# Optimization experiments

Measured on AMD Instinct MI355X. Metric: run time of the kernel, lower is better.

The kernel has to match this reference:

```python
import jax, jax.numpy as jnp
import numpy as np

B, T, D, H, L, F = 256, 32, 1024, 8, 3, 2048
SSRC, NCOL, NTAB, NACT, NSYM = 64, 32, 16, 64, 32
HD = D // H


def setup_inputs() -> dict:
    key = jax.random.key(0)
    ks = jax.random.split(key, 40)
    n = lambda k, s, sc=0.02: jax.random.normal(k, s, jnp.float32) * sc
    inp = {}
    inp["prev_action_emb"] = jax.random.normal(ks[0], (B, T, D), jnp.float32)
    inp["encoded_src"] = jax.random.normal(ks[1], (B, SSRC, D), jnp.float32)
    inp["encoded_col"] = jax.random.normal(ks[2], (B, NCOL, D), jnp.float32)
    inp["encoded_tab"] = jax.random.normal(ks[3], (B, NTAB, D), jnp.float32)
    inp["src_mask"] = jnp.zeros((B, SSRC), jnp.int32)  # 1 = padded
    inp["symbol_ids"] = jax.random.randint(ks[4], (B, T), 0, NSYM)
    inp["view_type"] = jax.random.randint(ks[5], (B,), 0, 3)  # 0=action,1=col,2=tab
    inp["gold_action"] = jax.random.randint(ks[6], (B,), 0, NACT)
    inp["gold_col"] = jax.random.randint(ks[7], (B,), 0, NCOL)
    inp["gold_tab"] = jax.random.randint(ks[8], (B,), 0, NTAB)
    # grammar embeddings (torch nn.Embedding default ~ N(0,1))
    inp["symbol_emb"] = jax.random.normal(ks[9], (NSYM, D), jnp.float32)
    inp["action_emb"] = jax.random.normal(ks[10], (NACT, D), jnp.float32)
    # affine heads
    inp["action_aff_w"] = n(ks[11], (D, D)); inp["action_aff_b"] = jnp.zeros((D,), jnp.float32)
    inp["symbol_aff_w"] = n(ks[12], (D, D)); inp["symbol_aff_b"] = jnp.zeros((D,), jnp.float32)
    inp["col_aff_w"] = n(ks[13], (D, D)); inp["col_aff_b"] = jnp.zeros((D,), jnp.float32)
    inp["tab_aff_w"] = n(ks[14], (D, D)); inp["tab_aff_b"] = jnp.zeros((D,), jnp.float32)
    inp["tgt_lin_w"] = n(ks[15], (2 * D, D)); inp["tgt_lin_b"] = jnp.zeros((D,), jnp.float32)
    inp["out_lin_w"] = n(ks[16], (D, D)); inp["out_lin_b"] = jnp.zeros((D,), jnp.float32)
    # transformer decoder layers (q,k,v,o stacked on axis 1)
    inp["self_w"] = n(ks[17], (L, 4, D, D)); inp["self_b"] = jnp.zeros((L, 4, D), jnp.float32)
    inp["cross_w"] = n(ks[18], (L, 4, D, D)); inp["cross_b"] = jnp.zeros((L, 4, D), jnp.float32)
    inp["ffn_w1"] = n(ks[19], (L, D, F)); inp["ffn_b1"] = jnp.zeros((L, F), jnp.float32)
    inp["ffn_w2"] = n(ks[20], (L, F, D)); inp["ffn_b2"] = jnp.zeros((L, D), jnp.float32)
    inp["ln_g"] = jnp.ones((L, 3, D), jnp.float32); inp["ln_b"] = jnp.zeros((L, 3, D), jnp.float32)
    return inp


def _pe(t, d):
    pos = jnp.arange(t, dtype=jnp.float32)[:, None]
    div = jnp.exp(jnp.arange(0, d, 2, dtype=jnp.float32) * (-np.log(10000.0) / d))
    pe = jnp.zeros((t, d), jnp.float32)
    pe = pe.at[:, 0::2].set(jnp.sin(pos * div)).at[:, 1::2].set(jnp.cos(pos * div))
    return pe


def _ln(x, g, b, eps=1e-5):
    m = jnp.mean(x, -1, keepdims=True)
    v = jnp.mean((x - m) ** 2, -1, keepdims=True)
    return (x - m) / jnp.sqrt(v + eps) * g + b


def _mha(xq, xkv, w, b, pad=None):
    # w: [4, D, D] for q,k,v,o; pad: [B, Tk] bool key-padding mask
    q = (xq @ w[0] + b[0]).reshape(xq.shape[0], -1, H, HD)
    k = (xkv @ w[1] + b[1]).reshape(xkv.shape[0], -1, H, HD)
    v = (xkv @ w[2] + b[2]).reshape(xkv.shape[0], -1, H, HD)
    s = jnp.einsum("bqhd,bkhd->bhqk", q, k) / np.sqrt(HD).astype(np.float32)
    if pad is not None:
        s = jnp.where(pad[:, None, None, :], -1e9, s)
    a = jax.nn.softmax(s, -1)
    o = jnp.einsum("bhqk,bkhd->bqhd", a, v).reshape(xq.shape[0], -1, D)
    return o @ w[3] + b[3]


def reference(prev_action_emb, encoded_src, encoded_col, encoded_tab, symbol_emb, action_emb,
              action_aff_w, action_aff_b, symbol_aff_w, symbol_aff_b, col_aff_w, col_aff_b,
              tab_aff_w, tab_aff_b, tgt_lin_w, tgt_lin_b, out_lin_w, out_lin_b,
              self_w, self_b, cross_w, cross_b, ffn_w1, ffn_b1, ffn_w2, ffn_b2, ln_g, ln_b,
              src_mask, symbol_ids, view_type, gold_action, gold_col, gold_tab):
    # target embeddings: affine(prev action emb) ++ affine(symbol emb gather)
    tgt_a = prev_action_emb @ action_aff_w + action_aff_b            # [B,T,D]
    tgt_s = symbol_emb[symbol_ids] @ symbol_aff_w + symbol_aff_b     # [B,T,D]
    x = jnp.concatenate([tgt_a, tgt_s], -1) @ tgt_lin_w + tgt_lin_b  # [B,T,D]
    x = x + _pe(T, D)[None]  # positional encoding (dropout = eval identity)
    pad = src_mask.astype(bool)
    for l in range(L):  # post-LN TransformerDecoderLayer (torch default, relu FFN)
        x = _ln(x + _mha(x, x, self_w[l], self_b[l]), ln_g[l, 0], ln_b[l, 0])
        x = _ln(x + _mha(x, encoded_src, cross_w[l], cross_b[l], pad), ln_g[l, 1], ln_b[l, 1])
        ff = jax.nn.relu(x @ ffn_w1[l] + ffn_b1[l]) @ ffn_w2[l] + ffn_b2[l]
        x = _ln(x + ff, ln_g[l, 2], ln_b[l, 2])
    out = x[:, -1, :] @ out_lin_w + out_lin_b  # [B,D], last decode position
    # three routed prediction heads: affine(src) . out -> masked log_softmax
    src_a = action_emb @ action_aff_w + action_aff_b                 # [A,D]
    logp_a = jax.nn.log_softmax(out @ src_a.T, -1)                   # [B,A]
    src_c = encoded_col @ col_aff_w + col_aff_b                      # [B,Nc,D]
    logp_c = jax.nn.log_softmax(jnp.einsum("bnd,bd->bn", src_c, out), -1)
    src_t = encoded_tab @ tab_aff_w + tab_aff_b                      # [B,Nt,D]
    logp_t = jax.nn.log_softmax(jnp.einsum("bnd,bd->bn", src_t, out), -1)
    ga = jnp.take_along_axis(logp_a, gold_action[:, None], 1)[:, 0]
    gc = jnp.take_along_axis(logp_c, gold_col[:, None], 1)[:, 0]
    gt = jnp.take_along_axis(logp_t, gold_tab[:, None], 1)[:, 0]
    # grammar routing: each example's loss comes from exactly one view
    nll = -jnp.where(view_type == 0, ga, jnp.where(view_type == 1, gc, gt))  # [B]
    return nll
```

## Files before the change

### kernel.cpp

```cpp
#include <hip/hip_runtime.h>

typedef float  f32x4 __attribute__((ext_vector_type(4)));
typedef short  s16x8 __attribute__((ext_vector_type(8)));

__device__ __forceinline__ float b2f(short s) {
    return __uint_as_float(((unsigned)(unsigned short)s) << 16);
}
__device__ __forceinline__ short f2b(float f) {
    unsigned u = __float_as_uint(f);
    u = u + 0x7fffu + ((u >> 16) & 1u);
    return (short)(u >> 16);
}

__device__ __forceinline__ void gld_lds16(const short* g, short* l) {
    __builtin_amdgcn_global_load_lds(
        (const __attribute__((address_space(1))) unsigned int*)(const void*)g,
        (__attribute__((address_space(3))) unsigned int*)(void*)l,
        16, 0, 0);
}

#define S_VMCNT(N)  asm volatile("s_waitcnt vmcnt(" #N ")" ::: "memory")
#define S_LGKM0     asm volatile("s_waitcnt lgkmcnt(0)" ::: "memory")
#define SBAR        __builtin_amdgcn_s_barrier()
#define SCHED0      __builtin_amdgcn_sched_barrier(0)

template<int BM>
__global__ __launch_bounds__(512) void gemm_pipe(
    const short* __restrict__ A, const short* __restrict__ Bt,
    const float* __restrict__ bias,
    short* __restrict__ Cb,
    const short* __restrict__ res,
    const float* __restrict__ sym2, const int* __restrict__ sid,
    const float* __restrict__ pe,
    int M, int N, int K, int epi)
{
    constexpr int MF   = BM / 32;
    constexpr int ALW  = BM / 128;
    constexpr int BUFB = (BM + 256) * 64;
    __shared__ short lds[4 * (BM + 256) * 32];

    const int tid  = threadIdx.x;
    const int lane = tid & 63;
    const int wave = tid >> 6;

    int bid = blockIdx.x;
    int nwg = gridDim.x;
    if ((nwg & 7) == 0) { int q = nwg >> 3; bid = (bid & 7) * q + (bid >> 3); }
    const int nbx = N >> 8;
    const int m0 = (bid / nbx) * BM;
    const int n0 = (bid % nbx) * 256;

    const int wm = (wave >> 2) * (BM / 2);
    const int wn = (wave & 3) * 64;
    const int l15 = lane & 15, l4 = lane >> 4;

    f32x4 acc[MF][4];
#pragma unroll
    for (int m = 0; m < MF; m++)
#pragma unroll
        for (int n = 0; n < 4; n++)
#pragma unroll
            for (int j = 0; j < 4; j++) acc[m][n][j] = 0.f;

    int aoff[MF], boff[4];
#pragma unroll
    for (int m = 0; m < MF; m++) {
        int r = wm + m * 16 + l15;
        aoff[m] = r * 64 + ((l4 ^ ((r >> 1) & 3)) << 4);
    }
#pragma unroll
    for (int n = 0; n < 4; n++) {
        int r = wn + n * 16 + l15;
        boff[n] = BM * 64 + r * 64 + ((l4 ^ ((r >> 1) & 3)) << 4);
    }

    const int lrow = lane >> 2;
    const int lch  = (lane & 3) ^ ((lane >> 3) & 3);
    size_t agoff[ALW]; int aldo[ALW];
#pragma unroll
    for (int i = 0; i < ALW; i++) {
        int ar = wave * (BM / 8) + i * 16;
        agoff[i] = (size_t)(m0 + ar + lrow) * K + lch * 8;
        aldo[i]  = ar * 64;
    }
    size_t bgoff[2]; int bldo[2];
#pragma unroll
    for (int i = 0; i < 2; i++) {
        int br = wave * 32 + i * 16;
        bgoff[i] = (size_t)(n0 + br + lrow) * K + lch * 8;
        bldo[i]  = BM * 64 + br * 64;
    }

    char* lbase = (char*)lds;
    auto stage = [&](int kt) {
        char* lb = lbase + (kt & 3) * BUFB;
        const size_t ke = (size_t)kt * 32;
#pragma unroll
        for (int i = 0; i < ALW; i++)
            gld_lds16(A + agoff[i] + ke, (short*)(lb + aldo[i]));
#pragma unroll
        for (int i = 0; i < 2; i++)
            gld_lds16(Bt + bgoff[i] + ke, (short*)(lb + bldo[i]));
    };

    const int NT = K >> 5;
    stage(0); stage(1); stage(2);

    for (int t = 0; t < NT; t++) {
        if (t + 3 < NT) stage(t + 3);
        const int rem = NT - 1 - t;
        if (rem >= 3)      { if constexpr (ALW == 2) S_VMCNT(12); else S_VMCNT(9); }
        else if (rem == 2) { if constexpr (ALW == 2) S_VMCNT(8);  else S_VMCNT(6); }
        else if (rem == 1) { if constexpr (ALW == 2) S_VMCNT(4);  else S_VMCNT(3); }
        else               S_VMCNT(0);
        SCHED0; SBAR; SCHED0;

        const char* cp = lbase + (t & 3) * BUFB;
        s16x8 af[MF], bv[4];
#pragma unroll
        for (int m = 0; m < MF; m++) af[m] = *(const s16x8*)(cp + aoff[m]);
#pragma unroll
        for (int n = 0; n < 4; n++)  bv[n] = *(const s16x8*)(cp + boff[n]);
        __builtin_amdgcn_s_setprio(1);
#pragma unroll
        for (int m = 0; m < MF; m++)
#pragma unroll
            for (int n = 0; n < 4; n++)
                acc[m][n] = __builtin_amdgcn_mfma_f32_16x16x32_bf16(
                    af[m], bv[n], acc[m][n], 0, 0, 0);
        __builtin_amdgcn_s_setprio(0);
        S_LGKM0; SCHED0; SBAR; SCHED0;
    }

#pragma unroll
    for (int m = 0; m < MF; m++) {
#pragma unroll
        for (int n = 0; n < 4; n++) {
#pragma unroll
            for (int j = 0; j < 4; j++) {
                int row = m0 + wm + m * 16 + l4 * 4 + j;
                int col = n0 + wn + n * 16 + l15;
                float v = acc[m][n][j];
                if (bias) v += bias[col];
                size_t idx = (size_t)row * N + col;
                if (epi == 0) {
                    Cb[idx] = f2b(v);
                } else if (epi == 2) {
                    v += sym2[(size_t)sid[row] * 1024 + col] + pe[(size_t)(row & 31) * 1024 + col];
                    Cb[idx] = f2b(v);
                } else if (epi == 3) {
                    Cb[idx] = f2b(fmaxf(v, 0.f));
                } else {
                    Cb[idx] = f2b(v + b2f(res[idx]));
                }
            }
        }
    }
}

__global__ __launch_bounds__(256) void gemm_bt(
    const short* __restrict__ A, const short* __restrict__ Bt,
    const float* __restrict__ bias,
    float* __restrict__ Cf, short* __restrict__ Cb,
    const short* __restrict__ res,
    int M, int N, int K, int epi)
{
    __shared__ short As[128 * 64];
    __shared__ short Bs[128 * 64];
    const int tid  = threadIdx.x;
    const int lane = tid & 63;
    const int wave = tid >> 6;
    const int m0 = blockIdx.y * 128, n0 = blockIdx.x * 128;
    const int wm = (wave >> 1) * 64, wn = (wave & 1) * 64;
    const int l15 = lane & 15, l4 = lane >> 4;

    f32x4 acc[4][4];
#pragma unroll
    for (int m = 0; m < 4; m++)
#pragma unroll
        for (int n = 0; n < 4; n++)
#pragma unroll
            for (int j = 0; j < 4; j++) acc[m][n][j] = 0.f;

    const int srow = wave * 32 + (lane >> 3);
    const int scol = (lane & 7) * 8;
    const short* Ag = A  + (size_t)(m0 + srow) * K + scol;
    const short* Bg = Bt + (size_t)(n0 + srow) * K + scol;
    short* Al = As + (wave * 32) * 64;
    short* Bl = Bs + (wave * 32) * 64;

    for (int k0 = 0; k0 < K; k0 += 64) {
#pragma unroll
        for (int i = 0; i < 4; i++) {
            gld_lds16(Ag + (size_t)(i * 8) * K + k0, Al + i * 8 * 64);
            gld_lds16(Bg + (size_t)(i * 8) * K + k0, Bl + i * 8 * 64);
        }
        __syncthreads();
#pragma unroll
        for (int kk = 0; kk < 64; kk += 32) {
            s16x8 af[4], bfv[4];
#pragma unroll
            for (int m = 0; m < 4; m++)
                af[m] = *(const s16x8*)(As + (wm + m * 16 + l15) * 64 + kk + l4 * 8);
#pragma unroll
            for (int n = 0; n < 4; n++)
                bfv[n] = *(const s16x8*)(Bs + (wn + n * 16 + l15) * 64 + kk + l4 * 8);
#pragma unroll
            for (int m = 0; m < 4; m++)
#pragma unroll
                for (int n = 0; n < 4; n++)
                    acc[m][n] = __builtin_amdgcn_mfma_f32_16x16x32_bf16(
                        af[m], bfv[n], acc[m][n], 0, 0, 0);
        }
        __syncthreads();
    }

#pragma unroll
    for (int m = 0; m < 4; m++) {
#pragma unroll
        for (int n = 0; n < 4; n++) {
#pragma unroll
            for (int j = 0; j < 4; j++) {
                int row = m0 + wm + m * 16 + l4 * 4 + j;
                int col = n0 + wn + n * 16 + l15;
                float v = acc[m][n][j];
                if (bias) v += bias[col];
                size_t idx = (size_t)row * N + col;
                if (epi == 0) {
                    Cb[idx] = f2b(v);
                } else if (epi == 1) {
                    Cf[idx] = v;
                } else if (epi == 3) {
                    Cb[idx] = f2b(fmaxf(v, 0.f));
                } else if (epi == 6) {
                    Cb[idx] = f2b(v + b2f(res[idx]));
                } else {
                    Cf[idx] = v; Cb[idx] = f2b(v);
                }
            }
        }
    }
}

__global__ __launch_bounds__(256) void attn_self(const short* __restrict__ qkv,
                                                 short* __restrict__ o)
{
    const int b = blockIdx.x >> 3, h = blockIdx.x & 7;
    __shared__ short Q[32 * 128], Kk[32 * 128], Vv[32 * 128];
    __shared__ float S[32 * 32];
    const int tid = threadIdx.x;
    const size_t base = (size_t)b * 32 * 3072 + h * 128;
    for (int i = tid; i < 512; i += 256) {
        int r = i >> 4, c = (i & 15) * 8;
        size_t g = base + (size_t)r * 3072 + c;
        *(s16x8*)(Q  + r * 128 + c) = *(const s16x8*)(qkv + g);
        *(s16x8*)(Kk + r * 128 + c) = *(const s16x8*)(qkv + g + 1024);
        *(s16x8*)(Vv + r * 128 + c) = *(const s16x8*)(qkv + g + 2048);
    }
    __syncthreads();
    for (int i = tid; i < 1024; i += 256) {
        int r = i >> 5, c = i & 31;
        float s = 0.f;
        for (int d8 = 0; d8 < 16; d8++) {
            s16x8 qa = *(const s16x8*)(Q  + r * 128 + d8 * 8);
            s16x8 ka = *(const s16x8*)(Kk + c * 128 + d8 * 8);
#pragma unroll
            for (int j = 0; j < 8; j++) s += b2f(qa[j]) * b2f(ka[j]);
        }
        S[i] = s * 0.088388347648318447f;
    }
    __syncthreads();
    if (tid < 32) {
        float mx = -1e30f;
        for (int c = 0; c < 32; c++) mx = fmaxf(mx, S[tid * 32 + c]);
        float sum = 0.f;
        for (int c = 0; c < 32; c++) { float p = __expf(S[tid * 32 + c] - mx); S[tid * 32 + c] = p; sum += p; }
        float inv = 1.f / sum;
        for (int c = 0; c < 32; c++) S[tid * 32 + c] *= inv;
    }
    __syncthreads();
    for (int i = tid; i < 4096; i += 256) {
        int r = i >> 7, d = i & 127;
        float a = 0.f;
        for (int c = 0; c < 32; c++) a += S[r * 32 + c] * b2f(Vv[c * 128 + d]);
        o[(size_t)(b * 32 + r) * 1024 + h * 128 + d] = f2b(a);
    }
}

__global__ __launch_bounds__(256) void attn_cross(const short* __restrict__ q_,
                                                  const short* __restrict__ ckv,
                                                  const int* __restrict__ mask,
                                                  short* __restrict__ o)
{
    const int b = blockIdx.x >> 3, h = blockIdx.x & 7;
    __shared__ short Q[32 * 128], Kk[64 * 128], Vv[64 * 128];
    __shared__ float S[32 * 64];
    const int tid = threadIdx.x;
    for (int i = tid; i < 512; i += 256) {
        int r = i >> 4, c = (i & 15) * 8;
        *(s16x8*)(Q + r * 128 + c) = *(const s16x8*)(q_ + (size_t)(b * 32 + r) * 1024 + h * 128 + c);
    }
    for (int i = tid; i < 1024; i += 256) {
        int r = i >> 4, c = (i & 15) * 8;
        size_t g = (size_t)(b * 64 + r) * 2048 + h * 128 + c;
        *(s16x8*)(Kk + r * 128 + c) = *(const s16x8*)(ckv + g);
        *(s16x8*)(Vv + r * 128 + c) = *(const s16x8*)(ckv + g + 1024);
    }
    __syncthreads();
    for (int i = tid; i < 2048; i += 256) {
        int r = i >> 6, c = i & 63;
        float s = 0.f;
        for (int d8 = 0; d8 < 16; d8++) {
            s16x8 qa = *(const s16x8*)(Q  + r * 128 + d8 * 8);
            s16x8 ka = *(const s16x8*)(Kk + c * 128 + d8 * 8);
#pragma unroll
            for (int j = 0; j < 8; j++) s += b2f(qa[j]) * b2f(ka[j]);
        }
        s *= 0.088388347648318447f;
        if (mask[b * 64 + c] != 0) s = -1e9f;
        S[i] = s;
    }
    __syncthreads();
    if (tid < 32) {
        float mx = -1e30f;
        for (int c = 0; c < 64; c++) mx = fmaxf(mx, S[tid * 64 + c]);
        float sum = 0.f;
        for (int c = 0; c < 64; c++) { float p = __expf(S[tid * 64 + c] - mx); S[tid * 64 + c] = p; sum += p; }
        float inv = 1.f / sum;
        for (int c = 0; c < 64; c++) S[tid * 64 + c] *= inv;
    }
    __syncthreads();
    for (int i = tid; i < 4096; i += 256) {
        int r = i >> 7, d = i & 127;
        float a = 0.f;
        for (int c = 0; c < 64; c++) a += S[r * 64 + c] * b2f(Vv[c * 128 + d]);
        o[(size_t)(b * 32 + r) * 1024 + h * 128 + d] = f2b(a);
    }
}

__global__ __launch_bounds__(256) void attn_self_last(const short* __restrict__ q,
                                                      const short* __restrict__ kv,
                                                      short* __restrict__ out)
{
    __shared__ float qs[4][128];
    __shared__ float ps[4][32];
    const int wave = threadIdx.x >> 6, lane = threadIdx.x & 63;
    const int idx = blockIdx.x * 4 + wave;
    const int b = idx >> 3, h = idx & 7;
    for (int d = lane; d < 128; d += 64)
        qs[wave][d] = b2f(q[(size_t)b * 1024 + h * 128 + d]);
    __syncthreads();
    float s = -1e30f;
    if (lane < 32) {
        const short* kr = kv + (size_t)(b * 32 + lane) * 2048 + h * 128;
        float a = 0.f;
        for (int d = 0; d < 128; d += 8) {
            s16x8 kvv = *(const s16x8*)(kr + d);
#pragma unroll
            for (int j = 0; j < 8; j++) a += qs[wave][d + j] * b2f(kvv[j]);
        }
        s = a * 0.088388347648318447f;
    }
    float mx = s;
#pragma unroll
    for (int o = 1; o < 32; o <<= 1) mx = fmaxf(mx, __shfl_xor(mx, o));
    float p = (lane < 32) ? __expf(s - mx) : 0.f;
    float sum = p;
#pragma unroll
    for (int o = 1; o < 32; o <<= 1) sum += __shfl_xor(sum, o);
    if (lane < 32) ps[wave][lane] = p / sum;
    __syncthreads();
    for (int d = lane; d < 128; d += 64) {
        float a = 0.f;
        for (int j = 0; j < 32; j++)
            a += ps[wave][j] * b2f(kv[(size_t)(b * 32 + j) * 2048 + 1024 + h * 128 + d]);
        out[(size_t)b * 1024 + h * 128 + d] = f2b(a);
    }
}

__global__ __launch_bounds__(256) void attn_cross_last(const short* __restrict__ q,
                                                       const short* __restrict__ ckv,
                                                       const int* __restrict__ mask,
                                                       short* __restrict__ out)
{
    __shared__ float qs[4][128];
    __shared__ float ps[4][64];
    const int wave = threadIdx.x >> 6, lane = threadIdx.x & 63;
    const int idx = blockIdx.x * 4 + wave;
    const int b = idx >> 3, h = idx & 7;
    for (int d = lane; d < 128; d += 64)
        qs[wave][d] = b2f(q[(size_t)b * 1024 + h * 128 + d]);
    __syncthreads();
    const short* kr = ckv + (size_t)(b * 64 + lane) * 2048 + h * 128;
    float a = 0.f;
    for (int d = 0; d < 128; d += 8) {
        s16x8 kvv = *(const s16x8*)(kr + d);
#pragma unroll
        for (int j = 0; j < 8; j++) a += qs[wave][d + j] * b2f(kvv[j]);
    }
    float s = a * 0.088388347648318447f;
    if (mask[b * 64 + lane] != 0) s = -1e9f;
    float mx = s;
#pragma unroll
    for (int o = 1; o < 64; o <<= 1) mx = fmaxf(mx, __shfl_xor(mx, o));
    float p = __expf(s - mx);
    float sum = p;
#pragma unroll
    for (int o = 1; o < 64; o <<= 1) sum += __shfl_xor(sum, o);
    ps[wave][lane] = p / sum;
    __syncthreads();
    for (int d = lane; d < 128; d += 64) {
        float acc = 0.f;
        for (int j = 0; j < 64; j++)
            acc += ps[wave][j] * b2f(ckv[(size_t)(b * 64 + j) * 2048 + 1024 + h * 128 + d]);
        out[(size_t)b * 1024 + h * 128 + d] = f2b(acc);
    }
}

__global__ __launch_bounds__(128) void ln_rows_b(const short* __restrict__ X,
                                                 short* __restrict__ Y,
                                                 const float* __restrict__ g,
                                                 const float* __restrict__ bt)
{
    const int row = blockIdx.x, tid = threadIdx.x;
    s16x8 v = *(const s16x8*)(X + (size_t)row * 1024 + tid * 8);
    float f[8];
    float s = 0.f, q = 0.f;
#pragma unroll
    for (int j = 0; j < 8; j++) { f[j] = b2f(v[j]); s += f[j]; q += f[j] * f[j]; }
#pragma unroll
    for (int o = 1; o < 64; o <<= 1) { s += __shfl_xor(s, o); q += __shfl_xor(q, o); }
    __shared__ float ls[2], lq[2];
    if ((tid & 63) == 0) { ls[tid >> 6] = s; lq[tid >> 6] = q; }
    __syncthreads();
    s = ls[0] + ls[1];
    q = lq[0] + lq[1];
    const float mean = s * 0.0009765625f;
    const float var  = q * 0.0009765625f - mean * mean;
    const float rs = rsqrtf(var + 1e-5f);
    s16x8 ov;
#pragma unroll
    for (int j = 0; j < 8; j++) {
        int c = tid * 8 + j;
        ov[j] = f2b((f[j] - mean) * rs * g[c] + bt[c]);
    }
    *(s16x8*)(Y + (size_t)row * 1024 + tid * 8) = ov;
}

__global__ __launch_bounds__(256) void convf2b(const float* __restrict__ s,
                                               short* __restrict__ d, int n)
{
    int i = (blockIdx.x * 256 + threadIdx.x) * 8;
    if (i < n) {
        float4 a = *(const float4*)(s + i);
        float4 b = *(const float4*)(s + i + 4);
        s16x8 o;
        o[0] = f2b(a.x); o[1] = f2b(a.y); o[2] = f2b(a.z); o[3] = f2b(a.w);
        o[4] = f2b(b.x); o[5] = f2b(b.y); o[6] = f2b(b.z); o[7] = f2b(b.w);
        *(s16x8*)(d + i) = o;
    }
}

__global__ __launch_bounds__(256) void transpose_conv_b(const float* __restrict__ src0,
                                                        short* __restrict__ dst0,
                                                        int R, int C)
{
    const float* src = src0 + (size_t)blockIdx.z * R * C;
    short* dst = dst0 + (size_t)blockIdx.z * R * C;
    __shared__ float t[32][33];
    int c0 = blockIdx.x * 32, r0 = blockIdx.y * 32;
    int tx = threadIdx.x & 31, ty = threadIdx.x >> 5;
#pragma unroll
    for (int i = 0; i < 32; i += 8) t[ty + i][tx] = src[(size_t)(r0 + ty + i) * C + c0 + tx];
    __syncthreads();
#pragma unroll
    for (int i = 0; i < 32; i += 8) dst[(size_t)(c0 + ty + i) * R + r0 + tx] = f2b(t[tx][ty + i]);
}

__global__ __launch_bounds__(256) void pad_conv(const float* __restrict__ s,
                                                short* __restrict__ d, int src_rows)
{
    int i = blockIdx.x * 256 + threadIdx.x;
    int r = i >> 10;
    d[i] = (r < src_rows) ? f2b(s[i]) : (short)0;
}

__global__ __launch_bounds__(256) void pe_build(float* __restrict__ pe)
{
    int i = blockIdx.x * 256 + threadIdx.x;
    int t = i >> 10, d = i & 1023;
    int de = d & ~1;
    float ang = (float)t * expf((float)de * (-9.2103403719761836f / 1024.f));
    pe[i] = (d & 1) ? cosf(ang) : sinf(ang);
}

__global__ __launch_bounds__(256) void gather_last(const short* __restrict__ x,
                                                   short* __restrict__ xlast)
{
    int i = blockIdx.x * 256 + threadIdx.x;
    int b = i >> 10, d = i & 1023;
    xlast[i] = x[((size_t)(b * 32 + 31) << 10) + d];
}

__global__ __launch_bounds__(64) void head_final(
    const float* __restrict__ logits_a,
    const float* __restrict__ enc_col_f, const short* __restrict__ yc,
    const float* __restrict__ enc_tab_f, const short* __restrict__ yt,
    const float* __restrict__ outf,
    const float* __restrict__ col_b, const float* __restrict__ tab_b,
    const int* __restrict__ view, const int* __restrict__ ga,
    const int* __restrict__ gc, const int* __restrict__ gt,
    float* __restrict__ nll)
{
    const int b = blockIdx.x, lane = threadIdx.x;
    const int vt = view[b];
    if (vt == 0) {
        float x = logits_a[(size_t)b * 128 + lane];
        float mx = x;
#pragma unroll
        for (int o = 1; o < 64; o <<= 1) mx = fmaxf(mx, __shfl_xor(mx, o));
        float sum = __expf(x - mx);
#pragma unroll
        for (int o = 1; o < 64; o <<= 1) sum += __shfl_xor(sum, o);
        float lse = mx + logf(sum);
        float gl = __shfl(x, ga[b]);
        if (lane == 0) nll[b] = lse - gl;
    } else {
        const int nit = (vt == 1) ? 32 : 16;
        const float* enc = (vt == 1) ? (enc_col_f + (size_t)b * 32 * 1024)
                                     : (enc_tab_f + (size_t)b * 16 * 1024);
        const short* y   = (vt == 1) ? (yc + (size_t)b * 1024) : (yt + (size_t)b * 1024);
        const float* bb  = (vt == 1) ? col_b : tab_b;
        float bc = 0.f;
        for (int i = lane; i < 1024; i += 64) bc += bb[i] * outf[(size_t)b * 1024 + i];
#pragma unroll
        for (int o = 1; o < 64; o <<= 1) bc += __shfl_xor(bc, o);
        float logit = -1e30f;
        if (lane < nit) {
            float s = bc;
            const float* er = enc + (size_t)lane * 1024;
            for (int d8 = 0; d8 < 128; d8++) {
                s16x8 yv = *(const s16x8*)(y + d8 * 8);
                float4 e0 = *(const float4*)(er + d8 * 8);
                float4 e1 = *(const float4*)(er + d8 * 8 + 4);
                s += e0.x * b2f(yv[0]) + e0.y * b2f(yv[1]) + e0.z * b2f(yv[2]) + e0.w * b2f(yv[3])
                   + e1.x * b2f(yv[4]) + e1.y * b2f(yv[5]) + e1.z * b2f(yv[6]) + e1.w * b2f(yv[7]);
            }
            logit = s;
        }
        float mx = logit;
#pragma unroll
        for (int o = 1; o < 64; o <<= 1) mx = fmaxf(mx, __shfl_xor(mx, o));
        float sum = (lane < nit) ? __expf(logit - mx) : 0.f;
#pragma unroll
        for (int o = 1; o < 64; o <<= 1) sum += __shfl_xor(sum, o);
        float lse = mx + logf(sum);
        int g = (vt == 1) ? gc[b] : gt[b];
        float gl = __shfl(logit, g);
        if (lane == 0) nll[b] = lse - gl;
    }
}

extern "C" void kernel_launch(void* const* d_in, const int* in_sizes, int n_in,
                              void* d_out, int out_size, void* d_ws, size_t ws_size,
                              hipStream_t stream)
{
    const float* pa_f     = (const float*)d_in[0];
    const float* src_f    = (const float*)d_in[1];
    const float* colenc_f = (const float*)d_in[2];
    const float* tabenc_f = (const float*)d_in[3];
    const int*   src_mask = (const int*)d_in[4];
    const int*   sym_ids  = (const int*)d_in[5];
    const int*   view     = (const int*)d_in[6];
    const int*   gold_a   = (const int*)d_in[7];
    const int*   gold_c   = (const int*)d_in[8];
    const int*   gold_t   = (const int*)d_in[9];
    const float* sym_emb  = (const float*)d_in[10];
    const float* act_emb  = (const float*)d_in[11];
    const float* Aaff_w   = (const float*)d_in[12];
    const float* Aaff_b   = (const float*)d_in[13];
    const float* Saff_w   = (const float*)d_in[14];
    const float* Saff_b   = (const float*)d_in[15];
    const float* Caff_w   = (const float*)d_in[16];
    const float* Caff_b   = (const float*)d_in[17];
    const float* Taff_w   = (const float*)d_in[18];
    const float* Taff_b   = (const float*)d_in[19];
    const float* tgt_w    = (const float*)d_in[20];
    const float* tgt_b    = (const float*)d_in[21];
    const float* outw     = (const float*)d_in[22];
    const float* outbias  = (const float*)d_in[23];
    const float* self_w   = (const float*)d_in[24];
    const float* self_b   = (const float*)d_in[25];
    const float* cross_w  = (const float*)d_in[26];
    const float* cross_b  = (const float*)d_in[27];
    const float* f1w      = (const float*)d_in[28];
    const float* f1b      = (const float*)d_in[29];
    const float* f2w      = (const float*)d_in[30];
    const float* f2bb     = (const float*)d_in[31];
    const float* lng      = (const float*)d_in[32];
    const float* lnbt     = (const float*)d_in[33];
    float* nll = (float*)d_out;

    char* ws = (char*)d_ws;
    size_t off = 0;
    auto alloc = [&](size_t bytes) -> char* {
        off = (off + 255) & ~(size_t)255;
        char* p = ws + off; off += bytes; return p;
    };

    const size_t MB1 = (size_t)1024 * 1024;
    short* WAaff  = (short*)alloc(MB1 * 2);
    short* WSaff  = (short*)alloc(MB1 * 2);
    short* Wtop   = (short*)alloc(MB1 * 2);
    short* Wbot   = (short*)alloc(MB1 * 2);
    short* Wout   = (short*)alloc(MB1 * 2);
    short* Wcol   = (short*)alloc(MB1 * 2);
    short* Wtab   = (short*)alloc(MB1 * 2);
    short* Wself  = (short*)alloc(12 * MB1 * 2);
    short* Wcross = (short*)alloc(12 * MB1 * 2);
    short* Wf1a   = (short*)alloc(3 * 2 * MB1 * 2);
    short* Wf2a   = (short*)alloc(3 * 2 * MB1 * 2);

    short* src_bf   = (short*)alloc((size_t)16384 * 1024 * 2);
    short* sym_pad  = (short*)alloc((size_t)128 * 1024 * 2);
    short* act_pad  = (short*)alloc((size_t)128 * 1024 * 2);
    short* sa_out   = (short*)alloc((size_t)128 * 1024 * 2);
    float* sym2     = (float*)alloc((size_t)128 * 1024 * 4);
    float* pe       = (float*)alloc((size_t)32 * 1024 * 4);
    short* tgt_a    = (short*)alloc((size_t)8192 * 1024 * 2);
    short* x_bf     = (short*)alloc((size_t)8192 * 1024 * 2);
    short* tmpb     = (short*)alloc((size_t)8192 * 1024 * 2);
    short* arena    = (short*)alloc((size_t)16384 * 2048 * 2);
    short* xlast    = (short*)alloc((size_t)256 * 1024 * 2);
    float* outf     = (float*)alloc((size_t)256 * 1024 * 4);
    short* outb16   = (short*)alloc((size_t)256 * 1024 * 2);
    short* srca     = (short*)alloc((size_t)128 * 1024 * 2);
    float* logits_a = (float*)alloc((size_t)256 * 128 * 4);
    short* ycb      = (short*)alloc((size_t)256 * 1024 * 2);
    short* ytb      = (short*)alloc((size_t)256 * 1024 * 2);
    short* xq31     = (short*)alloc((size_t)256 * 1024 * 2);
    short* x256a    = (short*)alloc((size_t)256 * 1024 * 2);
    short* x256b    = (short*)alloc((size_t)256 * 1024 * 2);
    short* q256     = (short*)alloc((size_t)256 * 1024 * 2);
    short* cq256    = (short*)alloc((size_t)256 * 1024 * 2);
    short* o256     = (short*)alloc((size_t)256 * 1024 * 2);
    short* h256     = (short*)alloc((size_t)256 * 2048 * 2);
    short* tmpb256  = (short*)alloc((size_t)256 * 1024 * 2);

    short* pa_bf = tmpb;
    short* cq    = tmpb;
    short* attn  = tgt_a;

    const dim3 BLK(256);
    auto conv = [&](const float* s, short* d, size_t n) {
        convf2b<<<dim3((unsigned)(n / 8 / 256)), BLK, 0, stream>>>(s, d, (int)n);
    };
    auto trans = [&](const float* s, short* d, int R, int C, int nm) {
        transpose_conv_b<<<dim3(C / 32, R / 32, nm), BLK, 0, stream>>>(s, d, R, C);
    };
    auto gp = [&](const short* A, const short* Bt, const float* bias,
                  short* Cb, const short* res,
                  const float* sy, const int* si, const float* pp,
                  int M, int N, int K, int epi, int BM) {
        if (BM == 256)
            gemm_pipe<256><<<dim3((N / 256) * (M / 256)), dim3(512), 0, stream>>>(
                A, Bt, bias, Cb, res, sy, si, pp, M, N, K, epi);
        else
            gemm_pipe<128><<<dim3((N / 256) * (M / 128)), dim3(512), 0, stream>>>(
                A, Bt, bias, Cb, res, sy, si, pp, M, N, K, epi);
    };
    auto gsm = [&](const short* A, const short* Bt, const float* bias,
                   float* Cf, short* Cb, const short* res,
                   int M, int N, int K, int epi) {
        gemm_bt<<<dim3(N / 128, M / 128), BLK, 0, stream>>>(
            A, Bt, bias, Cf, Cb, res, M, N, K, epi);
    };

    pe_build<<<dim3(128), BLK, 0, stream>>>(pe);
    conv(pa_f, pa_bf, (size_t)8192 * 1024);
    conv(src_f, src_bf, (size_t)16384 * 1024);
    conv(Caff_w, Wcol, MB1);
    conv(Taff_w, Wtab, MB1);
    pad_conv<<<dim3(512), BLK, 0, stream>>>(sym_emb, sym_pad, 32);
    pad_conv<<<dim3(512), BLK, 0, stream>>>(act_emb, act_pad, 64);
    trans(Aaff_w, WAaff, 1024, 1024, 1);
    trans(Saff_w, WSaff, 1024, 1024, 1);
    trans(tgt_w, Wtop, 1024, 1024, 1);
    trans(tgt_w + MB1, Wbot, 1024, 1024, 1);
    trans(outw, Wout, 1024, 1024, 1);
    trans(self_w, Wself, 1024, 1024, 12);
    trans(cross_w, Wcross, 1024, 1024, 12);
    trans(f1w, Wf1a, 1024, 2048, 3);
    trans(f2w, Wf2a, 2048, 1024, 3);

    gsm(sym_pad, WSaff, Saff_b, nullptr, sa_out, nullptr, 128, 1024, 1024, 0);
    gsm(sa_out, Wbot, nullptr, sym2, nullptr, nullptr, 128, 1024, 1024, 1);
    gp(pa_bf, WAaff, Aaff_b, tgt_a, nullptr, nullptr, nullptr, nullptr,
       8192, 1024, 1024, 0, 128);
    gp(tgt_a, Wtop, tgt_b, x_bf, nullptr, sym2, sym_ids, pe,
       8192, 1024, 1024, 2, 128);

    for (int l = 0; l < 2; l++) {
        const float* sb = self_b + (size_t)l * 4096;
        const float* cb = cross_b + (size_t)l * 4096;
        gp(x_bf, Wself + (size_t)(4 * l) * MB1, sb, arena, nullptr, nullptr, nullptr, nullptr,
           8192, 3072, 1024, 0, 256);
        attn_self<<<dim3(2048), BLK, 0, stream>>>(arena, attn);
        gp(attn, Wself + (size_t)(4 * l + 3) * MB1, sb + 3072, tmpb, x_bf, nullptr, nullptr, nullptr,
           8192, 1024, 1024, 6, 128);
        ln_rows_b<<<dim3(8192), dim3(128), 0, stream>>>(tmpb, x_bf,
            lng + (size_t)(l * 3 + 0) * 1024, lnbt + (size_t)(l * 3 + 0) * 1024);
        gp(x_bf, Wcross + (size_t)(4 * l) * MB1, cb, cq, nullptr, nullptr, nullptr, nullptr,
           8192, 1024, 1024, 0, 128);
        gp(src_bf, Wcross + (size_t)(4 * l + 1) * MB1, cb + 1024, arena, nullptr, nullptr, nullptr, nullptr,
           16384, 2048, 1024, 0, 256);
        attn_cross<<<dim3(2048), BLK, 0, stream>>>(cq, arena, src_mask, attn);
        gp(attn, Wcross + (size_t)(4 * l + 3) * MB1, cb + 3072, tmpb, x_bf, nullptr, nullptr, nullptr,
           8192, 1024, 1024, 6, 128);
        ln_rows_b<<<dim3(8192), dim3(128), 0, stream>>>(tmpb, x_bf,
            lng + (size_t)(l * 3 + 1) * 1024, lnbt + (size_t)(l * 3 + 1) * 1024);
        gp(x_bf, Wf1a + (size_t)l * 2 * MB1, f1b + (size_t)l * 2048, arena, nullptr, nullptr, nullptr, nullptr,
           8192, 2048, 1024, 3, 256);
        gp(arena, Wf2a + (size_t)l * 2 * MB1, f2bb + (size_t)l * 1024, tmpb, x_bf, nullptr, nullptr, nullptr,
           8192, 1024, 2048, 6, 128);
        ln_rows_b<<<dim3(8192), dim3(128), 0, stream>>>(tmpb, x_bf,
            lng + (size_t)(l * 3 + 2) * 1024, lnbt + (size_t)(l * 3 + 2) * 1024);
    }

    {
        const float* sb = self_b + (size_t)2 * 4096;
        const float* cb = cross_b + (size_t)2 * 4096;
        gather_last<<<dim3(1024), BLK, 0, stream>>>(x_bf, xq31);
        gp(x_bf, Wself + (size_t)(4 * 2 + 1) * MB1, sb + 1024, arena, nullptr, nullptr, nullptr, nullptr,
           8192, 2048, 1024, 0, 256);
        gsm(xq31, Wself + (size_t)(4 * 2) * MB1, sb, nullptr, q256, nullptr, 256, 1024, 1024, 0);
        attn_self_last<<<dim3(512), BLK, 0, stream>>>(q256, arena, o256);
        gsm(o256, Wself + (size_t)(4 * 2 + 3) * MB1, sb + 3072, nullptr, tmpb256, xq31, 256, 1024, 1024, 6);
        ln_rows_b<<<dim3(256), dim3(128), 0, stream>>>(tmpb256, x256a,
            lng + (size_t)(2 * 3 + 0) * 1024, lnbt + (size_t)(2 * 3 + 0) * 1024);
        gsm(x256a, Wcross + (size_t)(4 * 2) * MB1, cb, nullptr, cq256, nullptr, 256, 1024, 1024, 0);
        gp(src_bf, Wcross + (size_t)(4 * 2 + 1) * MB1, cb + 1024, arena, nullptr, nullptr, nullptr, nullptr,
           16384, 2048, 1024, 0, 256);
        attn_cross_last<<<dim3(512), BLK, 0, stream>>>(cq256, arena, src_mask, o256);
        gsm(o256, Wcross + (size_t)(4 * 2 + 3) * MB1, cb + 3072, nullptr, tmpb256, x256a, 256, 1024, 1024, 6);
        ln_rows_b<<<dim3(256), dim3(128), 0, stream>>>(tmpb256, x256b,
            lng + (size_t)(2 * 3 + 1) * 1024, lnbt + (size_t)(2 * 3 + 1) * 1024);
        gsm(x256b, Wf1a + (size_t)2 * 2 * MB1, f1b + (size_t)2 * 2048, nullptr, h256, nullptr,
            256, 2048, 1024, 3);
        gsm(h256, Wf2a + (size_t)2 * 2 * MB1, f2bb + (size_t)2 * 1024, nullptr, tmpb256, x256b,
            256, 1024, 2048, 6);
        ln_rows_b<<<dim3(256), dim3(128), 0, stream>>>(tmpb256, xlast,
            lng + (size_t)(2 * 3 + 2) * 1024, lnbt + (size_t)(2 * 3 + 2) * 1024);
    }

    gsm(xlast, Wout, outbias, outf, outb16, nullptr, 256, 1024, 1024, 5);
    gsm(act_pad, WAaff, Aaff_b, nullptr, srca, nullptr, 128, 1024, 1024, 0);
    gsm(outb16, srca, nullptr, logits_a, nullptr, nullptr, 256, 128, 1024, 1);
    gsm(outb16, Wcol, nullptr, nullptr, ycb, nullptr, 256, 1024, 1024, 0);
    gsm(outb16, Wtab, nullptr, nullptr, ytb, nullptr, 256, 1024, 1024, 0);
    head_final<<<dim3(256), dim3(64), 0, stream>>>(
        logits_a, colenc_f, ycb, tabenc_f, ytb, outf,
        Caff_b, Taff_b, view, gold_a, gold_c, gold_t, nll);
}
```

Baseline: 2.647 ms.

## Rewrite pipelined bf16 GEMM with 64-wide K tiles and phased LDS ping-pong

The main bf16 GEMM kernel goes from a 4-deep ring of 32-wide K tiles to 64-wide K tiles. It uses double buffering for BM=256 and triple buffering for BM=128, with an XOR-swizzled 128-byte LDS row layout. Each K step is split into quarter or half phases, and global-to-LDS loads for the next tile are issued between MFMA phases. The goal is fewer barrier and wait rounds per unit of MFMA work and better overlap of loads with compute. The cost is more barriers per iteration and a more intricate vmcnt schedule that is easy to get wrong.

```diff
diff --git a/kernel.cpp b/kernel.cpp
--- a/kernel.cpp
+++ b/kernel.cpp
@@ -25,7 +25,7 @@
 #define SCHED0      __builtin_amdgcn_sched_barrier(0)
 
 template<int BM>
-__global__ __launch_bounds__(512) void gemm_pipe(
+__global__ __launch_bounds__(512) void gemm8(
     const short* __restrict__ A, const short* __restrict__ Bt,
     const float* __restrict__ bias,
     short* __restrict__ Cb,
@@ -35,13 +35,14 @@
     int M, int N, int K, int epi)
 {
     constexpr int MF   = BM / 32;
-    constexpr int ALW  = BM / 128;
-    constexpr int BUFB = (BM + 256) * 64;
-    __shared__ short lds[4 * (BM + 256) * 32];
+    constexpr int BUF  = (BM + 256) * 128;
+    constexpr int NBUF = (BM == 256) ? 2 : 3;
+    constexpr int BOFS = BM * 128;
+    __shared__ __align__(16) char lds[NBUF * BUF];
 
     const int tid  = threadIdx.x;
     const int lane = tid & 63;
-    const int wave = tid >> 6;
+    const int w    = tid >> 6;
 
     int bid = blockIdx.x;
     int nwg = gridDim.x;
@@ -50,9 +51,9 @@
     const int m0 = (bid / nbx) * BM;
     const int n0 = (bid % nbx) * 256;
 
-    const int wm = (wave >> 2) * (BM / 2);
-    const int wn = (wave & 3) * 64;
-    const int l15 = lane & 15, l4 = lane >> 4;
+    const int wm = (w >> 2) * (BM / 2);
+    const int wn = (w & 3) * 64;
+    const int l15 = lane & 15, l4 = lane >> 4, key = lane & 7;
 
     f32x4 acc[MF][4];
 #pragma unroll
@@ -62,74 +63,98 @@
 #pragma unroll
             for (int j = 0; j < 4; j++) acc[m][n][j] = 0.f;
 
-    int aoff[MF], boff[4];
-#pragma unroll
-    for (int m = 0; m < MF; m++) {
-        int r = wm + m * 16 + l15;
-        aoff[m] = r * 64 + ((l4 ^ ((r >> 1) & 3)) << 4);
-    }
-#pragma unroll
-    for (int n = 0; n < 4; n++) {
-        int r = wn + n * 16 + l15;
-        boff[n] = BM * 64 + r * 64 + ((l4 ^ ((r >> 1) & 3)) << 4);
-    }
-
-    const int lrow = lane >> 2;
-    const int lch  = (lane & 3) ^ ((lane >> 3) & 3);
-    size_t agoff[ALW]; int aldo[ALW];
-#pragma unroll
-    for (int i = 0; i < ALW; i++) {
-        int ar = wave * (BM / 8) + i * 16;
-        agoff[i] = (size_t)(m0 + ar + lrow) * K + lch * 8;
-        aldo[i]  = ar * 64;
-    }
-    size_t bgoff[2]; int bldo[2];
-#pragma unroll
-    for (int i = 0; i < 2; i++) {
-        int br = wave * 32 + i * 16;
-        bgoff[i] = (size_t)(n0 + br + lrow) * K + lch * 8;
-        bldo[i]  = BM * 64 + br * 64;
-    }
-
-    char* lbase = (char*)lds;
-    auto stage = [&](int kt) {
-        char* lb = lbase + (kt & 3) * BUFB;
-        const size_t ke = (size_t)kt * 32;
-#pragma unroll
-        for (int i = 0; i < ALW; i++)
-            gld_lds16(A + agoff[i] + ke, (short*)(lb + aldo[i]));
-#pragma unroll
-        for (int i = 0; i < 2; i++)
-            gld_lds16(Bt + bgoff[i] + ke, (short*)(lb + bldo[i]));
-    };
-
-    const int NT = K >> 5;
-    stage(0); stage(1); stage(2);
-
-    for (int t = 0; t < NT; t++) {
-        if (t + 3 < NT) stage(t + 3);
-        const int rem = NT - 1 - t;
-        if (rem >= 3)      { if constexpr (ALW == 2) S_VMCNT(12); else S_VMCNT(9); }
-        else if (rem == 2) { if constexpr (ALW == 2) S_VMCNT(8);  else S_VMCNT(6); }
-        else if (rem == 1) { if constexpr (ALW == 2) S_VMCNT(4);  else S_VMCNT(3); }
-        else               S_VMCNT(0);
-        SCHED0; SBAR; SCHED0;
-
-        const char* cp = lbase + (t & 3) * BUFB;
-        s16x8 af[MF], bv[4];
-#pragma unroll
-        for (int m = 0; m < MF; m++) af[m] = *(const s16x8*)(cp + aoff[m]);
-#pragma unroll
-        for (int n = 0; n < 4; n++)  bv[n] = *(const s16x8*)(cp + boff[n]);
-        __builtin_amdgcn_s_setprio(1);
-#pragma unroll
-        for (int m = 0; m < MF; m++)
-#pragma unroll
-            for (int n = 0; n < 4; n++)
-                acc[m][n] = __builtin_amdgcn_mfma_f32_16x16x32_bf16(
-                    af[m], bv[n], acc[m][n], 0, 0, 0);
-        __builtin_amdgcn_s_setprio(0);
-        S_LGKM0; SCHED0; SBAR; SCHED0;
+    const int aof = (wm + l15) * 128 + ((l4 ^ key) << 4);
+    const int bof = BOFS + (wn + l15) * 128 + ((l4 ^ key) << 4);
+
+    const int r3 = lane >> 3;
+    const int sc = key ^ r3;
+    const int rsA = (BM == 256) ? ((w >> 2) * 128 + (w & 3) * 16) : (w * 16);
+    const short* Ag = A  + (size_t)(m0 + rsA + r3) * K + sc * 8;
+    const short* Bg = Bt + (size_t)(n0 + w * 16 + r3) * K + sc * 8;
+    const int ldA = rsA * 128;
+    const int ldB = BOFS + w * 16 * 128;
+
+    auto stgA = [&](int h, int t, char* lb) {
+#pragma unroll
+        for (int j = 0; j < 2; j++)
+            gld_lds16(Ag + (size_t)(h * 64 + j * 8) * K + (size_t)t * 64,
+                      (short*)(lb + ldA + h * 8192 + j * 1024));
+    };
+    auto stgB = [&](int h, int t, char* lb) {
+#pragma unroll
+        for (int j = 0; j < 2; j++)
+            gld_lds16(Bg + (size_t)(h * 128 + j * 8) * K + (size_t)t * 64,
+                      (short*)(lb + ldB + h * 16384 + j * 1024));
+    };
+    auto rdA = [&](const char* rb, int Q, int k, s16x8* av) {
+        const int o = (aof ^ (k ? 64 : 0)) + Q * 8192;
+#pragma unroll
+        for (int mf = 0; mf < 4; mf++) av[mf] = *(const s16x8*)(rb + o + mf * 2048);
+    };
+    auto rdB = [&](const char* rb, int k, s16x8* bv) {
+        const int o = bof ^ (k ? 64 : 0);
+#pragma unroll
+        for (int nf = 0; nf < 4; nf++) bv[nf] = *(const s16x8*)(rb + o + nf * 2048);
+    };
+    auto mm = [&](int Q, s16x8* av, s16x8* bv) {
+#pragma unroll
+        for (int mf = 0; mf < 4; mf++)
+#pragma unroll
+            for (int nf = 0; nf < 4; nf++)
+                acc[Q * 4 + mf][nf] = __builtin_amdgcn_mfma_f32_16x16x32_bf16(
+                    av[mf], bv[nf], acc[Q * 4 + mf][nf], 0, 0, 0);
+    };
+
+    const int NT = K >> 6;
+
+    if constexpr (BM == 256) {
+        stgA(0, 0, lds); stgB(0, 0, lds); stgA(1, 0, lds); stgB(1, 0, lds);
+        stgA(0, 1, lds + BUF); stgB(0, 1, lds + BUF);
+        S_VMCNT(4); SCHED0; SBAR; SCHED0;
+        for (int t = 0; t < NT; t++) {
+            char* rb = lds + (t & 1) * BUF;
+            char* ob = lds + ((t & 1) ^ 1) * BUF;
+            s16x8 av[4], bv[4];
+            rdA(rb, 0, 0, av); rdB(rb, 0, bv);
+            if (t + 1 < NT) { stgA(1, t + 1, ob); stgB(1, t + 1, ob); }
+            SBAR; S_LGKM0; SCHED0;
+            __builtin_amdgcn_s_setprio(1); mm(0, av, bv); __builtin_amdgcn_s_setprio(0);
+            SCHED0; SBAR;
+            rdA(rb, 1, 0, av);
+            SBAR; S_LGKM0; SCHED0;
+            __builtin_amdgcn_s_setprio(1); mm(1, av, bv); __builtin_amdgcn_s_setprio(0);
+            SCHED0; SBAR;
+            rdA(rb, 0, 1, av); rdB(rb, 1, bv);
+            SBAR; S_LGKM0; SCHED0;
+            __builtin_amdgcn_s_setprio(1); mm(0, av, bv); __builtin_amdgcn_s_setprio(0);
+            SCHED0; SBAR;
+            rdA(rb, 1, 1, av);
+            if (t + 2 < NT)      { stgA(0, t + 2, rb); stgB(0, t + 2, rb); S_VMCNT(4); }
+            else if (t + 1 < NT) { S_VMCNT(0); }
+            SBAR; S_LGKM0; SCHED0;
+            __builtin_amdgcn_s_setprio(1); mm(1, av, bv); __builtin_amdgcn_s_setprio(0);
+            SCHED0; SBAR;
+        }
+    } else {
+        char* c0 = lds; char* c1 = lds + BUF; char* c2 = lds + 2 * BUF;
+        stgA(0, 0, c0); stgB(0, 0, c0); stgB(1, 0, c0);
+        stgA(0, 1, c1); stgB(0, 1, c1); stgB(1, 1, c1);
+        S_VMCNT(6); SCHED0; SBAR; SCHED0;
+        for (int t = 0; t < NT; t++) {
+            s16x8 av[4], bv[4];
+            rdA(c0, 0, 0, av); rdB(c0, 0, bv);
+            if (t + 2 < NT) { stgA(0, t + 2, c2); stgB(0, t + 2, c2); }
+            SBAR; S_LGKM0; SCHED0;
+            __builtin_amdgcn_s_setprio(1); mm(0, av, bv); __builtin_amdgcn_s_setprio(0);
+            SCHED0; SBAR;
+            rdA(c0, 0, 1, av); rdB(c0, 1, bv);
+            if (t + 2 < NT)      { stgB(1, t + 2, c2); S_VMCNT(6); }
+            else if (t + 1 < NT) { S_VMCNT(0); }
+            SBAR; S_LGKM0; SCHED0;
+            __builtin_amdgcn_s_setprio(1); mm(0, av, bv); __builtin_amdgcn_s_setprio(0);
+            SCHED0; SBAR;
+            char* tb = c0; c0 = c1; c1 = c2; c2 = tb;
+        }
     }
 
 #pragma unroll
@@ -663,10 +688,10 @@
                   const float* sy, const int* si, const float* pp,
                   int M, int N, int K, int epi, int BM) {
         if (BM == 256)
-            gemm_pipe<256><<<dim3((N / 256) * (M / 256)), dim3(512), 0, stream>>>(
+            gemm8<256><<<dim3((N / 256) * (M / 256)), dim3(512), 0, stream>>>(
                 A, Bt, bias, Cb, res, sy, si, pp, M, N, K, epi);
         else
-            gemm_pipe<128><<<dim3((N / 256) * (M / 128)), dim3(512), 0, stream>>>(
+            gemm8<128><<<dim3((N / 256) * (M / 128)), dim3(512), 0, stream>>>(
                 A, Bt, bias, Cb, res, sy, si, pp, M, N, K, epi);
     };
     auto gsm = [&](const short* A, const short* Bt, const float* bias,
```

Measured after the change: 2.577 ms. 2.6% less time.

## Replace LDS-staged GEMM pipeline with direct global-to-register double-buffered loads

Applied to the files above, without the earlier changes.

The main bf16 GEMM no longer stages A/B tiles through LDS with global_load_lds and a 4-deep ring buffer. Each wave now loads its MFMA fragments straight from global memory into registers and ping-pongs between two register buffers. This removes LDS traffic and the block barriers. In exchange there is no data sharing across waves, so every wave re-reads the same A and B tiles from global/L2, and each lane issues 16-byte loads strided by K, which coalesces poorly.

```diff
diff --git a/kernel.cpp b/kernel.cpp
--- a/kernel.cpp
+++ b/kernel.cpp
@@ -19,13 +19,8 @@
         16, 0, 0);
 }
 
-#define S_VMCNT(N)  asm volatile("s_waitcnt vmcnt(" #N ")" ::: "memory")
-#define S_LGKM0     asm volatile("s_waitcnt lgkmcnt(0)" ::: "memory")
-#define SBAR        __builtin_amdgcn_s_barrier()
-#define SCHED0      __builtin_amdgcn_sched_barrier(0)
-
 template<int BM>
-__global__ __launch_bounds__(512) void gemm_pipe(
+__global__ __launch_bounds__(512) void gemm_reg(
     const short* __restrict__ A, const short* __restrict__ Bt,
     const float* __restrict__ bias,
     short* __restrict__ Cb,
@@ -34,14 +29,11 @@
     const float* __restrict__ pe,
     int M, int N, int K, int epi)
 {
-    constexpr int MF   = BM / 32;
-    constexpr int ALW  = BM / 128;
-    constexpr int BUFB = (BM + 256) * 64;
-    __shared__ short lds[4 * (BM + 256) * 32];
+    constexpr int MF = BM / 32;
 
     const int tid  = threadIdx.x;
     const int lane = tid & 63;
-    const int wave = tid >> 6;
+    const int w    = tid >> 6;
 
     int bid = blockIdx.x;
     int nwg = gridDim.x;
@@ -50,8 +42,8 @@
     const int m0 = (bid / nbx) * BM;
     const int n0 = (bid % nbx) * 256;
 
-    const int wm = (wave >> 2) * (BM / 2);
-    const int wn = (wave & 3) * 64;
+    const int wm = (w >> 2) * (BM / 2);
+    const int wn = (w & 3) * 64;
     const int l15 = lane & 15, l4 = lane >> 4;
 
     f32x4 acc[MF][4];
@@ -62,74 +54,55 @@
 #pragma unroll
             for (int j = 0; j < 4; j++) acc[m][n][j] = 0.f;
 
-    int aoff[MF], boff[4];
-#pragma unroll
-    for (int m = 0; m < MF; m++) {
-        int r = wm + m * 16 + l15;
-        aoff[m] = r * 64 + ((l4 ^ ((r >> 1) & 3)) << 4);
-    }
-#pragma unroll
-    for (int n = 0; n < 4; n++) {
-        int r = wn + n * 16 + l15;
-        boff[n] = BM * 64 + r * 64 + ((l4 ^ ((r >> 1) & 3)) << 4);
-    }
-
-    const int lrow = lane >> 2;
-    const int lch  = (lane & 3) ^ ((lane >> 3) & 3);
-    size_t agoff[ALW]; int aldo[ALW];
-#pragma unroll
-    for (int i = 0; i < ALW; i++) {
-        int ar = wave * (BM / 8) + i * 16;
-        agoff[i] = (size_t)(m0 + ar + lrow) * K + lch * 8;
-        aldo[i]  = ar * 64;
-    }
-    size_t bgoff[2]; int bldo[2];
-#pragma unroll
-    for (int i = 0; i < 2; i++) {
-        int br = wave * 32 + i * 16;
-        bgoff[i] = (size_t)(n0 + br + lrow) * K + lch * 8;
-        bldo[i]  = BM * 64 + br * 64;
-    }
-
-    char* lbase = (char*)lds;
-    auto stage = [&](int kt) {
-        char* lb = lbase + (kt & 3) * BUFB;
-        const size_t ke = (size_t)kt * 32;
-#pragma unroll
-        for (int i = 0; i < ALW; i++)
-            gld_lds16(A + agoff[i] + ke, (short*)(lb + aldo[i]));
-#pragma unroll
-        for (int i = 0; i < 2; i++)
-            gld_lds16(Bt + bgoff[i] + ke, (short*)(lb + bldo[i]));
-    };
-
-    const int NT = K >> 5;
-    stage(0); stage(1); stage(2);
-
-    for (int t = 0; t < NT; t++) {
-        if (t + 3 < NT) stage(t + 3);
-        const int rem = NT - 1 - t;
-        if (rem >= 3)      { if constexpr (ALW == 2) S_VMCNT(12); else S_VMCNT(9); }
-        else if (rem == 2) { if constexpr (ALW == 2) S_VMCNT(8);  else S_VMCNT(6); }
-        else if (rem == 1) { if constexpr (ALW == 2) S_VMCNT(4);  else S_VMCNT(3); }
-        else               S_VMCNT(0);
-        SCHED0; SBAR; SCHED0;
-
-        const char* cp = lbase + (t & 3) * BUFB;
-        s16x8 af[MF], bv[4];
-#pragma unroll
-        for (int m = 0; m < MF; m++) af[m] = *(const s16x8*)(cp + aoff[m]);
-#pragma unroll
-        for (int n = 0; n < 4; n++)  bv[n] = *(const s16x8*)(cp + boff[n]);
-        __builtin_amdgcn_s_setprio(1);
+    const short* aP[MF];
+    const short* bP[4];
+#pragma unroll
+    for (int m = 0; m < MF; m++)
+        aP[m] = A + (size_t)(m0 + wm + m * 16 + l15) * K + l4 * 8;
+#pragma unroll
+    for (int n = 0; n < 4; n++)
+        bP[n] = Bt + (size_t)(n0 + wn + n * 16 + l15) * K + l4 * 8;
+
+    s16x8 a0[MF], b0[4], a1[MF], b1[4];
+
+    auto ld0 = [&](int t) {
+        const int o = t * 32;
+#pragma unroll
+        for (int m = 0; m < MF; m++) a0[m] = *(const s16x8*)(aP[m] + o);
+#pragma unroll
+        for (int n = 0; n < 4; n++)  b0[n] = *(const s16x8*)(bP[n] + o);
+    };
+    auto ld1 = [&](int t) {
+        const int o = t * 32;
+#pragma unroll
+        for (int m = 0; m < MF; m++) a1[m] = *(const s16x8*)(aP[m] + o);
+#pragma unroll
+        for (int n = 0; n < 4; n++)  b1[n] = *(const s16x8*)(bP[n] + o);
+    };
+    auto mm0 = [&]() {
 #pragma unroll
         for (int m = 0; m < MF; m++)
 #pragma unroll
             for (int n = 0; n < 4; n++)
                 acc[m][n] = __builtin_amdgcn_mfma_f32_16x16x32_bf16(
-                    af[m], bv[n], acc[m][n], 0, 0, 0);
-        __builtin_amdgcn_s_setprio(0);
-        S_LGKM0; SCHED0; SBAR; SCHED0;
+                    a0[m], b0[n], acc[m][n], 0, 0, 0);
+    };
+    auto mm1 = [&]() {
+#pragma unroll
+        for (int m = 0; m < MF; m++)
+#pragma unroll
+            for (int n = 0; n < 4; n++)
+                acc[m][n] = __builtin_amdgcn_mfma_f32_16x16x32_bf16(
+                    a1[m], b1[n], acc[m][n], 0, 0, 0);
+    };
+
+    const int NT = K >> 5;
+    ld0(0);
+    for (int t = 0; t < NT; t += 2) {
+        if (t + 1 < NT) ld1(t + 1);
+        mm0();
+        if (t + 2 < NT) ld0(t + 2);
+        if (t + 1 < NT) mm1();
     }
 
 #pragma unroll
@@ -663,10 +636,10 @@
                   const float* sy, const int* si, const float* pp,
                   int M, int N, int K, int epi, int BM) {
         if (BM == 256)
-            gemm_pipe<256><<<dim3((N / 256) * (M / 256)), dim3(512), 0, stream>>>(
+            gemm_reg<256><<<dim3((N / 256) * (M / 256)), dim3(512), 0, stream>>>(
                 A, Bt, bias, Cb, res, sy, si, pp, M, N, K, epi);
         else
-            gemm_pipe<128><<<dim3((N / 256) * (M / 128)), dim3(512), 0, stream>>>(
+            gemm_reg<128><<<dim3((N / 256) * (M / 128)), dim3(512), 0, stream>>>(
                 A, Bt, bias, Cb, res, sy, si, pp, M, N, K, epi);
     };
     auto gsm = [&](const short* A, const short* Bt, const float* bias,
```

Result: slower. 4.746 ms (+79.3%).
